# Kernel optimization log

Measured on AMD Instinct MI355X. Metric: run time of the kernel, lower is better.

The kernel has to match this reference:

```python
import jax, jax.numpy as jnp
import numpy as np

NUM_TOKEN = 1024
IN_DIM = 512
OUT_DIM = 512
E = 1024          # expansion_factor * in_token_dims
S = 128
EPS = 1e-5
SQRT_S = float(np.sqrt(S))


def _rope_seq(x):
    """RoPE over axis 1 (sequence), last axis is feature dim. x: [B, L, ..., D]."""
    L = x.shape[1]
    half = x.shape[-1] // 2
    pos = jnp.arange(L, dtype=jnp.float32)
    inv_freq = 10000.0 ** (jnp.arange(half, dtype=jnp.float32) / half)
    sinusoid = pos[:, None] * inv_freq[None, :]          # [L, half]
    bshape = (1, L) + (1,) * (x.ndim - 3) + (half,)
    sin = jnp.sin(sinusoid).reshape(bshape)
    cos = jnp.cos(sinusoid).reshape(bshape)
    x1, x2 = jnp.split(x, 2, axis=-1)
    return jnp.concatenate([x1 * cos - x2 * sin, x2 * cos + x1 * sin], axis=-1)


def setup_inputs() -> dict:
    key = jax.random.key(0)
    ks = jax.random.split(key, 8)
    B = 32
    x = jax.random.normal(ks[0], (B, NUM_TOKEN, IN_DIM), jnp.float32)
    uv_w = jax.random.normal(ks[1], (2 * E + S, IN_DIM), jnp.float32) / np.sqrt(IN_DIM)
    o_w = jax.random.normal(ks[2], (OUT_DIM, E), jnp.float32) / np.sqrt(E)
    gamma = jax.random.uniform(ks[3], (2, S), jnp.float32)
    beta = jax.random.uniform(ks[4], (2, S), jnp.float32)
    w = jax.random.uniform(ks[5], (2 * NUM_TOKEN - 1,), jnp.float32)
    g = jnp.ones((1,), jnp.float32)                       # ScaleNorm gain
    res_scale = jnp.ones((IN_DIM,), jnp.float32)
    layer_scale = jnp.ones((OUT_DIM,), jnp.float32)
    return dict(x=x, uv_w=uv_w, o_w=o_w, gamma=gamma, beta=beta, w=w,
                g=g, res_scale=res_scale, layer_scale=layer_scale)


def reference(x, uv_w, o_w, gamma, beta, w, g, res_scale, layer_scale):
    B, L, D = x.shape
    # ScaleNorm
    norm = jnp.linalg.norm(x, axis=-1, keepdims=True) * (D ** -0.5)
    xn = x / jnp.maximum(norm, EPS) * g
    # shift mixing (time shift: first half channels shifted right by 1 token)
    xs, xp = jnp.split(xn, 2, axis=-1)
    xs = jnp.pad(xs, ((0, 0), (1, 0), (0, 0)))[:, :L, :]
    xn = jnp.concatenate([xs, xp], axis=-1)
    # uv projection + SiLU, then split into u, v, base
    uv = jax.nn.silu(xn @ uv_w.T)                         # [B, L, 2E+S]
    u, v, base = jnp.split(uv, [E, 2 * E], axis=-1)
    # per-head affine then RoPE
    base = base[:, :, None, :] * gamma[None, None] + beta  # [B, L, 2, S]
    base = _rope_seq(base)
    q, k = base[:, :, 0, :], base[:, :, 1, :]
    qk = jnp.einsum('bls,bms->blm', q, k)                 # [B, L, L]
    # structure-mode relative position bias: bias[i, j] = w[j - i + L - 1]
    idx = jnp.arange(L)[None, :] - jnp.arange(L)[:, None] + (L - 1)
    qk = qk + w[idx][None]
    kernel = jnp.square(jax.nn.relu(qk / SQRT_S))
    out = u * jnp.einsum('blm,bme->ble', kernel, v)       # gated quadratic attn
    out = out @ o_w.T                                     # [B, L, OUT_DIM]
    return x * res_scale + out * layer_scale
```

## Files before the change

### kernel.cpp

```cpp
#include <hip/hip_runtime.h>
#include <hip/hip_bf16.h>
#include <math.h>

typedef unsigned short u16;
typedef __bf16 bf16x8 __attribute__((ext_vector_type(8)));
typedef float f32x4 __attribute__((ext_vector_type(4)));

#define NB 32
#define LSEQ 1024
#define DIN 512
#define EDIM 1024
#define SDIM 128
#define NTOK (NB * LSEQ)
#define NUV 2176

#define AS1 __attribute__((address_space(1)))
#define AS3 __attribute__((address_space(3)))

__device__ __forceinline__ u16 f2bf(float f) {
  unsigned u = __builtin_bit_cast(unsigned, f);
  u += 0x7fffu + ((u >> 16) & 1u);
  return (u16)(u >> 16);
}
__device__ __forceinline__ float bf2f(u16 h) {
  unsigned u = ((unsigned)h) << 16;
  return __builtin_bit_cast(float, u);
}
__device__ __forceinline__ float fast_silu(float x) {
  float t = __builtin_amdgcn_exp2f(-1.44269504088896f * x);
  return x * __builtin_amdgcn_rcpf(1.0f + t);
}


__global__ __launch_bounds__(256) void k_f32_to_bf16(const float* __restrict__ in,
                                                     u16* __restrict__ out, int n4) {
  int i = blockIdx.x * 256 + threadIdx.x;
  if (i < n4) {
    float4 f = ((const float4*)in)[i];
    ushort4 o;
    o.x = f2bf(f.x); o.y = f2bf(f.y); o.z = f2bf(f.z); o.w = f2bf(f.w);
    ((ushort4*)out)[i] = o;
  }
}

__global__ __launch_bounds__(256) void k_normshift(const float* __restrict__ x,
                                                   const float* __restrict__ g,
                                                   u16* __restrict__ xn2) {
  int t = blockIdx.x;
  int l = t & (LSEQ - 1);
  float2 v = ((const float2*)(x + (size_t)t * DIN))[threadIdx.x];
  float ss = v.x * v.x + v.y * v.y;
  for (int o = 32; o > 0; o >>= 1) ss += __shfl_down(ss, o, 64);
  __shared__ float p[4];
  if ((threadIdx.x & 63) == 0) p[threadIdx.x >> 6] = ss;
  __syncthreads();
  float s = p[0] + p[1] + p[2] + p[3];
  float norm = sqrtf(s * (1.0f / (float)DIN));
  float inv = g[0] / fmaxf(norm, 1e-5f);
  int d = threadIdx.x * 2;
  ushort2 ob; ob.x = f2bf(v.x * inv); ob.y = f2bf(v.y * inv);
  if (d >= 256) {
    *(ushort2*)(xn2 + (size_t)t * DIN + d) = ob;
  } else {
    if (l < LSEQ - 1) *(ushort2*)(xn2 + (size_t)(t + 1) * DIN + d) = ob;
    if (l == 0) { ushort2 z = {0, 0}; *(ushort2*)(xn2 + (size_t)t * DIN + d) = z; }
  }
}

__global__ __launch_bounds__(256) void k_rope_table(float* __restrict__ sin_t,
                                                    float* __restrict__ cos_t) {
  int idx = blockIdx.x * 256 + threadIdx.x;
  int l = idx >> 6, j = idx & 63;
  double freq = pow(10000.0, (double)j / 64.0);
  float arg = (float)l * (float)freq;
  double a = (double)arg;
  sin_t[idx] = (float)sin(a);
  cos_t[idx] = (float)cos(a);
}

__global__ __launch_bounds__(256) void k_qkbuild(const u16* __restrict__ base,
                                                 const float* __restrict__ gamma,
                                                 const float* __restrict__ beta,
                                                 const float* __restrict__ sin_t,
                                                 const float* __restrict__ cos_t,
                                                 u16* __restrict__ q, u16* __restrict__ k) {
  int idx = blockIdx.x * 256 + threadIdx.x;
  int t = idx >> 6, j = idx & 63;
  int l = t & (LSEQ - 1);
  float b1 = bf2f(base[(size_t)t * SDIM + j]);
  float b2 = bf2f(base[(size_t)t * SDIM + j + 64]);
  float s = sin_t[l * 64 + j], c = cos_t[l * 64 + j];
  {
    float y1 = b1 * gamma[j] + beta[j];
    float y2 = b2 * gamma[64 + j] + beta[64 + j];
    q[(size_t)t * SDIM + j]      = f2bf(y1 * c - y2 * s);
    q[(size_t)t * SDIM + j + 64] = f2bf(y2 * c + y1 * s);
  }
  {
    float y1 = b1 * gamma[128 + j] + beta[128 + j];
    float y2 = b2 * gamma[192 + j] + beta[192 + j];
    k[(size_t)t * SDIM + j]      = f2bf(y1 * c - y2 * s);
    k[(size_t)t * SDIM + j + 64] = f2bf(y2 * c + y1 * s);
  }
}


#define GROW_A(s) (wr * 128 + (s) * 32 + wc * 8)
#define GROW_B(s) (wid * 32 + (s) * 8)

#define STG_PAIR(s, At2, Bt2, dA, dB)                                              \
  do {                                                                             \
    __builtin_amdgcn_global_load_lds(                                              \
        (AS1 unsigned int*)((At2) + (size_t)(GROW_A(s) + srow) * lda + scol),      \
        (AS3 unsigned int*)((dA) + GROW_A(s) * 64), 16, 0, 0);                     \
    __builtin_amdgcn_global_load_lds(                                              \
        (AS1 unsigned int*)((Bt2) + (size_t)(GROW_B(s) + srow) * ldb + scol),      \
        (AS3 unsigned int*)((dB) + GROW_B(s) * 64), 16, 0, 0);                     \
  } while (0)

#define RD_A(dst, cbuf, q)                                                         \
  do {                                                                             \
    _Pragma("unroll") for (int r_ = 0; r_ < 2; ++r_)                               \
    _Pragma("unroll") for (int h_ = 0; h_ < 2; ++h_)                               \
      dst[r_][h_] = *(const bf16x8*)((cbuf) + (wr * 128 + (q) * 32 + r_ * 16 + fr) * 64 + \
                                     (((h_ * 4 + kg) ^ fr7) * 8));                 \
  } while (0)

#define RD_B(cbuf)                                                                 \
  do {                                                                             \
    _Pragma("unroll") for (int n_ = 0; n_ < 4; ++n_)                               \
    _Pragma("unroll") for (int h_ = 0; h_ < 2; ++h_)                               \
      breg[n_][h_] = *(const bf16x8*)((cbuf) + (wc * 64 + n_ * 16 + fr) * 64 +     \
                                      (((h_ * 4 + kg) ^ fr7) * 8));                \
  } while (0)

#define MFMA16(s, areg)                                                            \
  do {                                                                             \
    __builtin_amdgcn_s_setprio(1);                                                 \
    _Pragma("unroll") for (int r_ = 0; r_ < 2; ++r_)                               \
    _Pragma("unroll") for (int n_ = 0; n_ < 4; ++n_)                               \
    _Pragma("unroll") for (int h_ = 0; h_ < 2; ++h_)                               \
      acc[(s) * 2 + r_][n_] = __builtin_amdgcn_mfma_f32_16x16x32_bf16(             \
          areg[r_][h_], breg[n_][h_], acc[(s) * 2 + r_][n_], 0, 0, 0);             \
    __builtin_amdgcn_s_setprio(0);                                                 \
  } while (0)

#define BAR_FENCE()                                                                \
  do { __builtin_amdgcn_s_barrier(); asm volatile("" ::: "memory"); } while (0)

__device__ __forceinline__ void gemm256p_core(const u16* __restrict__ A, int lda,
                                              const u16* __restrict__ B, int ldb,
                                              int K, u16* smem, f32x4 (&acc)[8][4]) {
  const int tid = threadIdx.x;
  const int lane = tid & 63, wid = tid >> 6;
  const int wr = wid >> 2, wc = wid & 3;
  const int fr = lane & 15, kg = lane >> 4, fr7 = fr & 7;
  const int srow = lane >> 3;
  const int scol = ((lane & 7) ^ srow) * 8;
  u16* cA = smem;
  u16* cB = smem + 16384;
  u16* nA = smem + 32768;
  u16* nB = smem + 49152;
  const int nt = K >> 6;

#pragma unroll
  for (int s = 0; s < 4; ++s) STG_PAIR(s, A, B, cA, cB);
#pragma unroll
  for (int s = 0; s < 4; ++s) STG_PAIR(s, A + 64, B + 64, nA, nB);
  asm volatile("s_waitcnt vmcnt(8)" ::: "memory");
  BAR_FENCE();

  bf16x8 breg[4][2], ac[2][2], an[2][2];
  RD_B(cB);
  RD_A(ac, cA, 0);

  for (int t = 0; t < nt; ++t) {
    const bool st = (t + 2) < nt;
    const u16* At2 = A + (size_t)(t + 2) * 64;
    const u16* Bt2 = B + (size_t)(t + 2) * 64;
    MFMA16(0, ac);
    RD_A(an, cA, 1);
    BAR_FENCE();
    if (st) STG_PAIR(0, At2, Bt2, cA, cB);
    MFMA16(1, an);
    RD_A(ac, cA, 2);
    BAR_FENCE();
    if (st) STG_PAIR(1, At2, Bt2, cA, cB);
    MFMA16(2, ac);
    RD_A(an, cA, 3);
    BAR_FENCE();
    if (st) STG_PAIR(2, At2, Bt2, cA, cB);
    MFMA16(3, an);
    if (st) asm volatile("s_waitcnt vmcnt(6)" ::: "memory");
    else    asm volatile("s_waitcnt vmcnt(0)" ::: "memory");
    BAR_FENCE();
    if (st) STG_PAIR(3, At2, Bt2, cA, cB);
    { u16* tp = cA; cA = nA; nA = tp; tp = cB; cB = nB; nB = tp; }
    if (t + 1 < nt) { RD_B(cB); RD_A(ac, cA, 0); }
  }
}

__global__ __launch_bounds__(512, 2) void k_gemm_uv(const u16* __restrict__ xn2,
                                                    const u16* __restrict__ wbf,
                                                    u16* __restrict__ u, u16* __restrict__ vt,
                                                    u16* __restrict__ base) {
  __shared__ __align__(16) u16 smem[65536];
  f32x4 acc[8][4] = {};
  int bid = blockIdx.x;
  int xcd = bid & 7;
  int off = bid >> 3;
  int m0 = (xcd * 16 + off / 9) * 256;
  int n0 = (off % 9) * 256;
  gemm256p_core(xn2 + (size_t)m0 * DIN, DIN, wbf + (size_t)n0 * DIN, DIN, DIN, smem, acc);
  int lane = threadIdx.x & 63, wid = threadIdx.x >> 6;
  int wr = wid >> 2, wc = wid & 3;
  int cb = n0 + wc * 64 + (lane & 15);
  int rb = m0 + wr * 128 + (lane >> 4) * 4;
  if (n0 < EDIM) {
#pragma unroll
    for (int mm = 0; mm < 8; ++mm)
#pragma unroll
      for (int n = 0; n < 4; ++n) {
        int c = cb + n * 16;
#pragma unroll
        for (int j = 0; j < 4; ++j) {
          int r = rb + mm * 16 + j;
          u[(size_t)r * EDIM + c] = f2bf(fast_silu(acc[mm][n][j]));
        }
      }
  } else if (n0 < 2 * EDIM) {
    int b = m0 >> 10;
    u16* vtb = vt + (size_t)b * (EDIM * LSEQ);
#pragma unroll
    for (int mm = 0; mm < 8; ++mm) {
      int l0 = (rb + mm * 16) & (LSEQ - 1);
#pragma unroll
      for (int n = 0; n < 4; ++n) {
        int e = cb + n * 16 - EDIM;
        ushort4 o;
        o.x = f2bf(fast_silu(acc[mm][n][0]));
        o.y = f2bf(fast_silu(acc[mm][n][1]));
        o.z = f2bf(fast_silu(acc[mm][n][2]));
        o.w = f2bf(fast_silu(acc[mm][n][3]));
        *(ushort4*)(vtb + (size_t)e * LSEQ + l0) = o;
      }
    }
  } else if (wc < 2) {
#pragma unroll
    for (int mm = 0; mm < 8; ++mm)
#pragma unroll
      for (int n = 0; n < 4; ++n) {
        int c = cb + n * 16 - 2 * EDIM;
#pragma unroll
        for (int j = 0; j < 4; ++j) {
          int r = rb + mm * 16 + j;
          base[(size_t)r * SDIM + c] = f2bf(fast_silu(acc[mm][n][j]));
        }
      }
  }
}

__global__ __launch_bounds__(512, 2) void k_attn(const u16* __restrict__ qg_,
                                                 const u16* __restrict__ kg_,
                                                 const u16* __restrict__ vtg,
                                                 const float* __restrict__ w,
                                                 u16* u_io) {
  __shared__ __align__(16) u16 smem[59648];
  u16* k0 = smem;            u16* k1 = smem + 8192;
  u16* v0 = smem + 16384;    u16* v1 = smem + 32768;
  u16* sS = smem + 49152;
  float* wwin = (float*)(smem + 57344);

  const int tid = threadIdx.x;
  const int lane = tid & 63, wid = tid >> 6;
  const int fr = lane & 15, kg = lane >> 4, fr7 = fr & 7;
  int bid = blockIdx.x;
  int xcd = bid & 7;
  int idx = bid >> 3;
  int b = xcd * 4 + (idx >> 5);
  int t5 = idx & 31;
  int m0 = (t5 >> 2) * 128;
  int e0 = (t5 & 3) * 256;
  const u16* qp = qg_ + (size_t)(b * LSEQ) * SDIM;
  const u16* kp = kg_ + (size_t)(b * LSEQ) * SDIM;
  const u16* vp = vtg + (size_t)b * LSEQ * EDIM + (size_t)e0 * LSEQ;

  if (tid < 288)
    __builtin_amdgcn_global_load_lds((AS1 unsigned int*)(w + (896 - m0) + tid * 4),
                                     (AS3 unsigned int*)(wwin + tid * 4), 16, 0, 0);

  bf16x8 qreg[4];
#pragma unroll
  for (int kf = 0; kf < 4; ++kf)
    qreg[kf] = *(const bf16x8*)(qp + (size_t)(m0 + wid * 16 + fr) * SDIM + kf * 32 + kg * 8);

  auto stage_k = [&](const u16* src_base, u16* dst) {
#pragma unroll
    for (int j2 = 0; j2 < 2; ++j2) {
      int ix = tid + j2 * 512;
      int row = ix >> 4, slot = ix & 15;
      int sslot = (slot & 8) | ((slot & 7) ^ (row & 7));
      __builtin_amdgcn_global_load_lds((AS1 unsigned int*)(src_base + (size_t)row * SDIM + sslot * 8),
                                       (AS3 unsigned int*)(dst + ix * 8), 16, 0, 0);
    }
  };
  auto stage_vt = [&](const u16* src_base, u16* dst) {
#pragma unroll
    for (int j2 = 0; j2 < 4; ++j2) {
      int ix = tid + j2 * 512;
      int row = ix >> 3, slot = (ix & 7) ^ (row & 7);
      __builtin_amdgcn_global_load_lds((AS1 unsigned int*)(src_base + (size_t)row * LSEQ + slot * 8),
                                       (AS3 unsigned int*)(dst + ix * 8), 16, 0, 0);
    }
  };

  stage_k(kp, k0);
  stage_vt(vp, v0);
  stage_k(kp + 64 * SDIM, k1);
  stage_vt(vp + 64, v1);
  asm volatile("s_waitcnt vmcnt(6)" ::: "memory");
  __builtin_amdgcn_sched_barrier(0);
  BAR_FENCE();

  const int wr = wid >> 2, wc = wid & 3;
  f32x4 acc[4][4] = {};
  const float inv_sqrt_s = 0.08838834764831845f;

  for (int t = 0; t < 16; ++t) {
    u16* kc = (t & 1) ? k1 : k0;
    u16* vc = (t & 1) ? v1 : v0;
    const bool st = t < 14;
    int l0 = t * 64;
    f32x4 sacc[4] = {};
#pragma unroll
    for (int n = 0; n < 4; ++n)
#pragma unroll
      for (int kf = 0; kf < 4; ++kf) {
        int sl = kf * 4 + kg;
        int sw = (sl & 8) | ((sl & 7) ^ fr7);
        bf16x8 kfr = *(const bf16x8*)(kc + (n * 16 + fr) * 128 + sw * 8);
        sacc[n] = __builtin_amdgcn_mfma_f32_16x16x32_bf16(qreg[kf], kfr, sacc[n], 0, 0, 0);
      }
    {
      int mbase = wid * 16 + kg * 4;
#pragma unroll
      for (int n = 0; n < 4; ++n) {
        int lloc = n * 16 + fr;
#pragma unroll
        for (int j = 0; j < 4; ++j) {
          int row = mbase + j;
          float val = (sacc[n][j] + wwin[l0 + lloc + 127 - row]) * inv_sqrt_s;
          val = fmaxf(val, 0.0f);
          int sw = (lloc >> 3) ^ (row & 7);
          sS[row * 64 + sw * 8 + (lloc & 7)] = f2bf(val * val);
        }
      }
    }
    asm volatile("s_waitcnt lgkmcnt(0)" ::: "memory");
    __builtin_amdgcn_sched_barrier(0);
    BAR_FENCE();
    if (st) stage_k(kp + (size_t)(l0 + 128) * SDIM, kc);
#pragma unroll
    for (int kh = 0; kh < 2; ++kh) {
      bf16x8 afr[4], bfr[4];
#pragma unroll
      for (int i = 0; i < 4; ++i) {
        int row = wr * 64 + i * 16 + fr;
        int sw = (kh * 4 + kg) ^ fr7;
        afr[i] = *(const bf16x8*)(sS + row * 64 + sw * 8);
      }
#pragma unroll
      for (int n = 0; n < 4; ++n) {
        int row = wc * 64 + n * 16 + fr;
        int sw = (kh * 4 + kg) ^ fr7;
        bfr[n] = *(const bf16x8*)(vc + row * 64 + sw * 8);
      }
      __builtin_amdgcn_s_setprio(1);
#pragma unroll
      for (int i = 0; i < 4; ++i)
#pragma unroll
        for (int n = 0; n < 4; ++n)
          acc[i][n] = __builtin_amdgcn_mfma_f32_16x16x32_bf16(afr[i], bfr[n], acc[i][n], 0, 0, 0);
      __builtin_amdgcn_s_setprio(0);
    }
    BAR_FENCE();
    if (st) stage_vt(vp + (l0 + 128), vc);
    if (st) asm volatile("s_waitcnt vmcnt(6)" ::: "memory");
    else    asm volatile("s_waitcnt vmcnt(0)" ::: "memory");
    __builtin_amdgcn_sched_barrier(0);
    BAR_FENCE();
  }

  int cb = e0 + wc * 64 + fr;
  int rb = m0 + wr * 64 + kg * 4;
#pragma unroll
  for (int i = 0; i < 4; ++i)
#pragma unroll
    for (int n = 0; n < 4; ++n) {
      int c = cb + n * 16;
#pragma unroll
      for (int j = 0; j < 4; ++j) {
        int r = rb + i * 16 + j;
        size_t ix = (size_t)(b * LSEQ + r) * EDIM + c;
        u_io[ix] = f2bf(acc[i][n][j] * bf2f(u_io[ix]));
      }
    }
}

__global__ __launch_bounds__(512, 2) void k_gemm_out(const u16* __restrict__ attn,
                                                     const u16* __restrict__ owbf,
                                                     const float* __restrict__ x,
                                                     const float* __restrict__ res_scale,
                                                     const float* __restrict__ layer_scale,
                                                     float* __restrict__ out) {
  __shared__ __align__(16) u16 smem[65536];
  f32x4 acc[8][4] = {};
  int bid = blockIdx.x;
  int xcd = bid & 7;
  int off = bid >> 3;
  int m0 = (xcd * 16 + (off >> 1)) * 256;
  int n0 = (off & 1) * 256;
  gemm256p_core(attn + (size_t)m0 * EDIM, EDIM, owbf + (size_t)n0 * EDIM, EDIM,
                EDIM, smem, acc);
  int lane = threadIdx.x & 63, wid = threadIdx.x >> 6;
  int wr = wid >> 2, wc = wid & 3;
  int cb = n0 + wc * 64 + (lane & 15);
  int rb = m0 + wr * 128 + (lane >> 4) * 4;
#pragma unroll
  for (int mm = 0; mm < 8; ++mm)
#pragma unroll
    for (int n = 0; n < 4; ++n) {
      int c = cb + n * 16;
#pragma unroll
      for (int j = 0; j < 4; ++j) {
        int r = rb + mm * 16 + j;
        out[(size_t)r * DIN + c] =
            x[(size_t)r * DIN + c] * res_scale[c] + acc[mm][n][j] * layer_scale[c];
      }
    }
}


extern "C" void kernel_launch(void* const* d_in, const int* in_sizes, int n_in,
                              void* d_out, int out_size, void* d_ws, size_t ws_size,
                              hipStream_t stream) {
  const float* x          = (const float*)d_in[0];
  const float* uv_w       = (const float*)d_in[1];
  const float* o_w        = (const float*)d_in[2];
  const float* gamma      = (const float*)d_in[3];
  const float* beta       = (const float*)d_in[4];
  const float* w          = (const float*)d_in[5];
  const float* g          = (const float*)d_in[6];
  const float* res_scale  = (const float*)d_in[7];
  const float* layer_scale= (const float*)d_in[8];
  float* out = (float*)d_out;

  char* ws = (char*)d_ws;
  u16* xn2    = (u16*)(ws + 0);
  u16* q      = (u16*)(ws + 0);
  u16* k      = (u16*)(ws + 8388608);
  u16* base   = (u16*)(ws + 33554432);
  u16* u_io   = (u16*)(ws + 50331648);
  u16* vt     = (u16*)(ws + 117440512);
  u16* uvw_bf = (u16*)(ws + 184549376);
  u16* ow_bf  = (u16*)(ws + 186908672);
  float* sin_t = (float*)(ws + 187957248);
  float* cos_t = (float*)(ws + 188219392);

  k_f32_to_bf16<<<dim3((NUV * DIN / 4 + 255) / 256), 256, 0, stream>>>(uv_w, uvw_bf, NUV * DIN / 4);
  k_f32_to_bf16<<<dim3((DIN * EDIM / 4 + 255) / 256), 256, 0, stream>>>(o_w, ow_bf, DIN * EDIM / 4);
  k_rope_table<<<dim3(LSEQ * 64 / 256), 256, 0, stream>>>(sin_t, cos_t);
  k_normshift<<<dim3(NTOK), 256, 0, stream>>>(x, g, xn2);

  k_gemm_uv<<<dim3(1152), 512, 0, stream>>>(xn2, uvw_bf, u_io, vt, base);

  k_qkbuild<<<dim3(NTOK * 64 / 256), 256, 0, stream>>>(base, gamma, beta, sin_t, cos_t, q, k);

  k_attn<<<dim3(1024), 512, 0, stream>>>(q, k, vt, w, u_io);

  k_gemm_out<<<dim3(256), 512, 0, stream>>>(u_io, ow_bf, x, res_scale, layer_scale, out);
}
```

Baseline: 362.0 us.

## Halve attention E-tile, single-buffer K, and raise k_attn occupancy to four blocks

The attention kernel's per-block E tile shrinks from 256 to 128 columns and the grid doubles. K staging moves to a single LDS buffer loaded one step ahead, which cuts LDS use enough to allow launch bounds of four blocks per CU instead of two. The score-matrix LDS swizzle also changes to use row>>1. The aim is more resident waves and better latency hiding, but every block now recomputes the QK^T scores, so score work doubles relative to the PV GEMM, and the register budget per thread tightens.

```diff
diff --git a/kernel.cpp b/kernel.cpp
--- a/kernel.cpp
+++ b/kernel.cpp
@@ -260,16 +260,16 @@
   }
 }
 
-__global__ __launch_bounds__(512, 2) void k_attn(const u16* __restrict__ qg_,
+__global__ __launch_bounds__(512, 4) void k_attn(const u16* __restrict__ qg_,
                                                  const u16* __restrict__ kg_,
                                                  const u16* __restrict__ vtg,
                                                  const float* __restrict__ w,
                                                  u16* u_io) {
-  __shared__ __align__(16) u16 smem[59648];
-  u16* k0 = smem;            u16* k1 = smem + 8192;
-  u16* v0 = smem + 16384;    u16* v1 = smem + 32768;
-  u16* sS = smem + 49152;
-  float* wwin = (float*)(smem + 57344);
+  __shared__ __align__(16) u16 smem[35072];
+  u16* kb = smem;
+  u16* v0 = smem + 8192;     u16* v1 = smem + 16384;
+  u16* sS = smem + 24576;
+  float* wwin = (float*)(smem + 32768);
 
   const int tid = threadIdx.x;
   const int lane = tid & 63, wid = tid >> 6;
@@ -277,36 +277,36 @@
   int bid = blockIdx.x;
   int xcd = bid & 7;
   int idx = bid >> 3;
-  int b = xcd * 4 + (idx >> 5);
-  int t5 = idx & 31;
-  int m0 = (t5 >> 2) * 128;
-  int e0 = (t5 & 3) * 256;
+  int b = xcd * 4 + (idx >> 6);
+  int t6 = idx & 63;
+  int m0 = (t6 >> 3) * 128;
+  int e0 = (t6 & 7) * 128;
   const u16* qp = qg_ + (size_t)(b * LSEQ) * SDIM;
   const u16* kp = kg_ + (size_t)(b * LSEQ) * SDIM;
   const u16* vp = vtg + (size_t)b * LSEQ * EDIM + (size_t)e0 * LSEQ;
 
+  bf16x8 qreg[4];
+#pragma unroll
+  for (int kf = 0; kf < 4; ++kf)
+    qreg[kf] = *(const bf16x8*)(qp + (size_t)(m0 + wid * 16 + fr) * SDIM + kf * 32 + kg * 8);
+
   if (tid < 288)
     __builtin_amdgcn_global_load_lds((AS1 unsigned int*)(w + (896 - m0) + tid * 4),
                                      (AS3 unsigned int*)(wwin + tid * 4), 16, 0, 0);
 
-  bf16x8 qreg[4];
-#pragma unroll
-  for (int kf = 0; kf < 4; ++kf)
-    qreg[kf] = *(const bf16x8*)(qp + (size_t)(m0 + wid * 16 + fr) * SDIM + kf * 32 + kg * 8);
-
-  auto stage_k = [&](const u16* src_base, u16* dst) {
+  auto stage_k = [&](const u16* src_base) {
 #pragma unroll
     for (int j2 = 0; j2 < 2; ++j2) {
       int ix = tid + j2 * 512;
       int row = ix >> 4, slot = ix & 15;
       int sslot = (slot & 8) | ((slot & 7) ^ (row & 7));
       __builtin_amdgcn_global_load_lds((AS1 unsigned int*)(src_base + (size_t)row * SDIM + sslot * 8),
-                                       (AS3 unsigned int*)(dst + ix * 8), 16, 0, 0);
+                                       (AS3 unsigned int*)(kb + ix * 8), 16, 0, 0);
     }
   };
   auto stage_vt = [&](const u16* src_base, u16* dst) {
 #pragma unroll
-    for (int j2 = 0; j2 < 4; ++j2) {
+    for (int j2 = 0; j2 < 2; ++j2) {
       int ix = tid + j2 * 512;
       int row = ix >> 3, slot = (ix & 7) ^ (row & 7);
       __builtin_amdgcn_global_load_lds((AS1 unsigned int*)(src_base + (size_t)row * LSEQ + slot * 8),
@@ -314,22 +314,19 @@
     }
   };
 
-  stage_k(kp, k0);
+  stage_k(kp);
   stage_vt(vp, v0);
-  stage_k(kp + 64 * SDIM, k1);
   stage_vt(vp + 64, v1);
-  asm volatile("s_waitcnt vmcnt(6)" ::: "memory");
+  asm volatile("s_waitcnt vmcnt(2)" ::: "memory");
   __builtin_amdgcn_sched_barrier(0);
   BAR_FENCE();
 
   const int wr = wid >> 2, wc = wid & 3;
-  f32x4 acc[4][4] = {};
+  f32x4 acc[4][2] = {};
   const float inv_sqrt_s = 0.08838834764831845f;
 
   for (int t = 0; t < 16; ++t) {
-    u16* kc = (t & 1) ? k1 : k0;
     u16* vc = (t & 1) ? v1 : v0;
-    const bool st = t < 14;
     int l0 = t * 64;
     f32x4 sacc[4] = {};
 #pragma unroll
@@ -338,7 +335,7 @@
       for (int kf = 0; kf < 4; ++kf) {
         int sl = kf * 4 + kg;
         int sw = (sl & 8) | ((sl & 7) ^ fr7);
-        bf16x8 kfr = *(const bf16x8*)(kc + (n * 16 + fr) * 128 + sw * 8);
+        bf16x8 kfr = *(const bf16x8*)(kb + (n * 16 + fr) * 128 + sw * 8);
         sacc[n] = __builtin_amdgcn_mfma_f32_16x16x32_bf16(qreg[kf], kfr, sacc[n], 0, 0, 0);
       }
     {
@@ -351,7 +348,7 @@
           int row = mbase + j;
           float val = (sacc[n][j] + wwin[l0 + lloc + 127 - row]) * inv_sqrt_s;
           val = fmaxf(val, 0.0f);
-          int sw = (lloc >> 3) ^ (row & 7);
+          int sw = (lloc >> 3) ^ ((row >> 1) & 7);
           sS[row * 64 + sw * 8 + (lloc & 7)] = f2bf(val * val);
         }
       }
@@ -359,44 +356,44 @@
     asm volatile("s_waitcnt lgkmcnt(0)" ::: "memory");
     __builtin_amdgcn_sched_barrier(0);
     BAR_FENCE();
-    if (st) stage_k(kp + (size_t)(l0 + 128) * SDIM, kc);
+    if (t + 1 < 16) stage_k(kp + (size_t)(l0 + 64) * SDIM);
 #pragma unroll
     for (int kh = 0; kh < 2; ++kh) {
-      bf16x8 afr[4], bfr[4];
+      bf16x8 afr[4], bfr[2];
 #pragma unroll
       for (int i = 0; i < 4; ++i) {
         int row = wr * 64 + i * 16 + fr;
-        int sw = (kh * 4 + kg) ^ fr7;
+        int sw = (kh * 4 + kg) ^ ((row >> 1) & 7);
         afr[i] = *(const bf16x8*)(sS + row * 64 + sw * 8);
       }
 #pragma unroll
-      for (int n = 0; n < 4; ++n) {
-        int row = wc * 64 + n * 16 + fr;
-        int sw = (kh * 4 + kg) ^ fr7;
+      for (int n = 0; n < 2; ++n) {
+        int row = wc * 32 + n * 16 + fr;
+        int sw = (kh * 4 + kg) ^ (fr & 7);
         bfr[n] = *(const bf16x8*)(vc + row * 64 + sw * 8);
       }
       __builtin_amdgcn_s_setprio(1);
 #pragma unroll
       for (int i = 0; i < 4; ++i)
 #pragma unroll
-        for (int n = 0; n < 4; ++n)
+        for (int n = 0; n < 2; ++n)
           acc[i][n] = __builtin_amdgcn_mfma_f32_16x16x32_bf16(afr[i], bfr[n], acc[i][n], 0, 0, 0);
       __builtin_amdgcn_s_setprio(0);
     }
     BAR_FENCE();
-    if (st) stage_vt(vp + (l0 + 128), vc);
-    if (st) asm volatile("s_waitcnt vmcnt(6)" ::: "memory");
-    else    asm volatile("s_waitcnt vmcnt(0)" ::: "memory");
+    if (t + 2 < 16) stage_vt(vp + (l0 + 128), vc);
+    if (t + 2 < 16) asm volatile("s_waitcnt vmcnt(2)" ::: "memory");
+    else            asm volatile("s_waitcnt vmcnt(0)" ::: "memory");
     __builtin_amdgcn_sched_barrier(0);
     BAR_FENCE();
   }
 
-  int cb = e0 + wc * 64 + fr;
+  int cb = e0 + wc * 32 + fr;
   int rb = m0 + wr * 64 + kg * 4;
 #pragma unroll
   for (int i = 0; i < 4; ++i)
 #pragma unroll
-    for (int n = 0; n < 4; ++n) {
+    for (int n = 0; n < 2; ++n) {
       int c = cb + n * 16;
 #pragma unroll
       for (int j = 0; j < 4; ++j) {
@@ -476,7 +473,7 @@
 
   k_qkbuild<<<dim3(NTOK * 64 / 256), 256, 0, stream>>>(base, gamma, beta, sin_t, cos_t, q, k);
 
-  k_attn<<<dim3(1024), 512, 0, stream>>>(q, k, vt, w, u_io);
+  k_attn<<<dim3(2048), 512, 0, stream>>>(q, k, vt, w, u_io);
 
   k_gemm_out<<<dim3(256), 512, 0, stream>>>(u_io, ow_bf, x, res_scale, layer_scale, out);
 }
```

New measurement: 390.2 us. 7.8% more time.
